# Kernel tuning notes

Measured on AMD Instinct MI355X. Metric: run time of the kernel, lower is better.

Reference implementation:

```python
import jax, jax.numpy as jnp
import numpy as np

N, D_IN, D_SAE, K = 8192, 768, 24576, 32


def setup_inputs() -> dict:
    key = jax.random.key(0)
    k1, k2, k3 = jax.random.split(key, 3)
    x = jax.random.normal(k1, (N, D_IN), dtype=jnp.float32)
    # kaiming_uniform_ on empty(d_in, d_sae): bound = sqrt(6 / d_in) (fan_in = d_sae? torch uses
    # fan_in = size(1) = d_sae for W_enc; we just need a same-scale random init for a reference)
    b_enc_bound = np.sqrt(6.0 / D_SAE)
    W_enc = jax.random.uniform(k2, (D_IN, D_SAE), dtype=jnp.float32,
                               minval=-b_enc_bound, maxval=b_enc_bound)
    b_dec_bound = np.sqrt(6.0 / D_IN)
    W_dec = jax.random.uniform(k3, (D_SAE, D_IN), dtype=jnp.float32,
                               minval=-b_dec_bound, maxval=b_dec_bound)
    # module normalizes decoder rows to unit L2 norm at init
    W_dec = W_dec / jnp.linalg.norm(W_dec, axis=1, keepdims=True)
    b_enc = jnp.zeros((D_SAE,), dtype=jnp.float32)
    b_dec = jnp.zeros((D_IN,), dtype=jnp.float32)
    return {"x": x, "W_enc": W_enc, "b_enc": b_enc, "W_dec": W_dec, "b_dec": b_dec}


def reference(x, W_enc, b_enc, W_dec, b_dec):
    # encode: relu((x - b_dec) @ W_enc + b_enc)
    z = jax.nn.relu((x - b_dec) @ W_enc + b_enc)            # [N, d_sae]
    topk_vals, topk_inds = jax.lax.top_k(z, K)              # [N, K]
    rows = jnp.arange(z.shape[0])[:, None]                  # [N, 1]
    z_sparse = jnp.zeros_like(z).at[rows, topk_inds].set(topk_vals)
    x_reconstruct = z_sparse @ W_dec + b_dec                # [N, d_in]
    return (x_reconstruct, z_sparse)
```

## Files before the change

### kernel.cpp

```cpp
#include <hip/hip_runtime.h>

#define N_ROWS 8192
#define D_IN   768
#define D_SAE  24576
#define K_TOP  32
#define C_SEL  40
#define DELTA  2e-4f

typedef __attribute__((ext_vector_type(8))) short bf16x8;
typedef __attribute__((ext_vector_type(4))) float f32x4;

__device__ __forceinline__ ushort f2bf(float f) {
    const unsigned u = __float_as_uint(f);
    return (ushort)((u + 0x7FFFu + ((u >> 16) & 1u)) >> 16);
}
__device__ __forceinline__ float bf2f(ushort h) {
    return __uint_as_float(((unsigned)h) << 16);
}

#define GBM 128
#define GBN 192
#define GBK 32

__global__ __launch_bounds__(256)
void sae_cvt_x(const float* __restrict__ x, const float* __restrict__ b_dec,
               ushort* __restrict__ ahi, ushort* __restrict__ alo)
{
    const int idx = blockIdx.x * 256 + threadIdx.x;
    const int i   = idx * 4;
    const int k   = (idx % (D_IN / 4)) * 4;
    const float4 xv = *(const float4*)(&x[i]);
    const float4 bd = *(const float4*)(&b_dec[k]);
    const float e[4] = {xv.x - bd.x, xv.y - bd.y, xv.z - bd.z, xv.w - bd.w};
    ushort h[4], l[4];
#pragma unroll
    for (int j = 0; j < 4; ++j) {
        h[j] = f2bf(e[j]);
        l[j] = f2bf(e[j] - bf2f(h[j]));
    }
    *(ushort4*)(&ahi[i]) = make_ushort4(h[0], h[1], h[2], h[3]);
    *(ushort4*)(&alo[i]) = make_ushort4(l[0], l[1], l[2], l[3]);
}

__global__ __launch_bounds__(256)
void sae_cvt_w(const float* __restrict__ W_enc,
               ushort* __restrict__ bhi, ushort* __restrict__ blo)
{
    __shared__ float tile[32][33];
    const int n0 = blockIdx.x * 32;
    const int k0 = blockIdx.y * 32;
    const int t  = threadIdx.x;
    const int r  = t >> 3;
    const int c4 = (t & 7) * 4;
    *(float4*)(&tile[r][c4]) = *(const float4*)(&W_enc[(size_t)(k0 + r) * D_SAE + n0 + c4]);
    __syncthreads();
    ushort h[4], l[4];
#pragma unroll
    for (int j = 0; j < 4; ++j) {
        const float e = tile[c4 + j][r];
        h[j] = f2bf(e);
        l[j] = f2bf(e - bf2f(h[j]));
    }
    *(ushort4*)(&bhi[(size_t)(n0 + r) * D_IN + k0 + c4]) = make_ushort4(h[0], h[1], h[2], h[3]);
    *(ushort4*)(&blo[(size_t)(n0 + r) * D_IN + k0 + c4]) = make_ushort4(l[0], l[1], l[2], l[3]);
}

__global__ __launch_bounds__(256, 2)
void sae_encode_mfma3(const ushort* __restrict__ ahi, const ushort* __restrict__ alo,
                      const ushort* __restrict__ bhi, const ushort* __restrict__ blo,
                      const float* __restrict__ b_enc, float* __restrict__ z)
{
    __shared__ ushort A_lds[2][4][GBM][8];
    __shared__ ushort B_lds[2][4][GBN][8];

    const int tid  = threadIdx.x;
    const int lane = tid & 63;
    const int wid  = tid >> 6;
    const int wr   = wid >> 1;
    const int wc   = wid & 1;
    const int l15  = lane & 15;
    const int lc   = lane >> 4;

    const int col0  = blockIdx.y * GBN;
    const int arow0 = blockIdx.x * GBM;
    const int row_w = arow0 + wr * 64;

    const int NT = D_IN / GBK;

    f32x4 acc[4][6];
#pragma unroll
    for (int i = 0; i < 4; ++i)
#pragma unroll
        for (int j = 0; j < 6; ++j) acc[i][j] = (f32x4){0.f, 0.f, 0.f, 0.f};

    bf16x8 s0, s1, s2, s3, s4, s5, s6, s7, s8, s9;

#define LOADQ(J, DST) { \
        const int q = (J) * 4 + wid; \
        if ((J) < 4) { \
            const int pl = q & 1, c = (q >> 1) & 3, h = q >> 3; \
            DST = *(const bf16x8*)((pl ? alo : ahi) + (size_t)(arow0 + h * 64 + lane) * D_IN + k0s + c * 8); \
        } else { \
            const int r2 = q - 16; \
            const int pl = r2 & 1, c = (r2 >> 1) & 3, g = r2 >> 3; \
            DST = *(const bf16x8*)((pl ? blo : bhi) + (size_t)(col0 + g * 64 + lane) * D_IN + k0s + c * 8); \
        } }

#define WRITEQ(J, SRC) { \
        const int q = (J) * 4 + wid; \
        if ((J) < 4) { \
            const int pl = q & 1, c = (q >> 1) & 3, h = q >> 3; \
            *(bf16x8*)(&A_lds[pl][c][h * 64 + lane][0]) = SRC; \
        } else { \
            const int r2 = q - 16; \
            const int pl = r2 & 1, c = (r2 >> 1) & 3, g = r2 >> 3; \
            *(bf16x8*)(&B_lds[pl][c][g * 64 + lane][0]) = SRC; \
        } }

#define LOAD_ALL() { LOADQ(0, s0) LOADQ(1, s1) LOADQ(2, s2) LOADQ(3, s3) LOADQ(4, s4) \
                     LOADQ(5, s5) LOADQ(6, s6) LOADQ(7, s7) LOADQ(8, s8) LOADQ(9, s9) }
#define WRITE_ALL() { WRITEQ(0, s0) WRITEQ(1, s1) WRITEQ(2, s2) WRITEQ(3, s3) WRITEQ(4, s4) \
                      WRITEQ(5, s5) WRITEQ(6, s6) WRITEQ(7, s7) WRITEQ(8, s8) WRITEQ(9, s9) }

    {
        const int k0s = 0;
        LOAD_ALL();
    }

    for (int kt = 0; kt < NT; ++kt) {
        WRITE_ALL();
        __syncthreads();

        if (kt + 1 < NT) {
            const int k0s = (kt + 1) * GBK;
            LOAD_ALL();
        }

        bf16x8 bh[6], bl[6];
#pragma unroll
        for (int ct = 0; ct < 6; ++ct) {
            const int n = wc * 96 + ct * 16 + l15;
            bh[ct] = *(const bf16x8*)(&B_lds[0][lc][n][0]);
            bl[ct] = *(const bf16x8*)(&B_lds[1][lc][n][0]);
        }
#pragma unroll
        for (int rt = 0; rt < 4; ++rt) {
            const int m = wr * 64 + rt * 16 + l15;
            const bf16x8 ah = *(const bf16x8*)(&A_lds[0][lc][m][0]);
            const bf16x8 al = *(const bf16x8*)(&A_lds[1][lc][m][0]);
#pragma unroll
            for (int ct = 0; ct < 6; ++ct) {
                acc[rt][ct] = __builtin_amdgcn_mfma_f32_16x16x32_bf16(ah, bh[ct], acc[rt][ct], 0, 0, 0);
                acc[rt][ct] = __builtin_amdgcn_mfma_f32_16x16x32_bf16(ah, bl[ct], acc[rt][ct], 0, 0, 0);
                acc[rt][ct] = __builtin_amdgcn_mfma_f32_16x16x32_bf16(al, bh[ct], acc[rt][ct], 0, 0, 0);
            }
        }
        __syncthreads();
    }

#undef LOAD_ALL
#undef WRITE_ALL
#undef LOADQ
#undef WRITEQ

#pragma unroll
    for (int ct = 0; ct < 6; ++ct) {
        const int col = col0 + wc * 96 + ct * 16 + l15;
        const float bec = b_enc[col];
#pragma unroll
        for (int rt = 0; rt < 4; ++rt) {
            const int rowb = row_w + rt * 16 + lc * 4;
#pragma unroll
            for (int r = 0; r < 4; ++r)
                z[(size_t)(rowb + r) * D_SAE + col] = fmaxf(acc[rt][ct][r] + bec, 0.f);
        }
    }
}

__global__ __launch_bounds__(256, 2)
void sae_encode_mfma(const float* __restrict__ x,
                     const float* __restrict__ W_enc,
                     const float* __restrict__ b_enc,
                     const float* __restrict__ b_dec,
                     float* __restrict__ z)
{
    __shared__ ushort Bs[2][4][GBN][8];

    const int tid  = threadIdx.x;
    const int lane = tid & 63;
    const int wid  = tid >> 6;
    const int wr   = wid >> 1;
    const int wc   = wid & 1;
    const int l15  = lane & 15;
    const int lc   = lane >> 4;

    const int col0  = blockIdx.x * GBN;
    const int row_w = blockIdx.y * GBM + wr * 64;

    f32x4 acc[4][6];
#pragma unroll
    for (int i = 0; i < 4; ++i)
#pragma unroll
        for (int j = 0; j < 6; ++j) acc[i][j] = (f32x4){0.f, 0.f, 0.f, 0.f};

    for (int kt = 0; kt < D_IN / GBK; ++kt) {
        const int k0 = kt * GBK;

        float bvv[3][8];
#pragma unroll
        for (int np = 0; np < 3; ++np)
#pragma unroll
            for (int it = 0; it < 8; ++it)
                bvv[np][it] = W_enc[(size_t)(k0 + wid * 8 + it) * D_SAE + col0 + np * 64 + lane];

        const float4 bd0 = *(const float4*)(&b_dec[k0 + lc * 8]);
        const float4 bd1 = *(const float4*)(&b_dec[k0 + lc * 8 + 4]);
        bf16x8 ah[4], al[4];
#pragma unroll
        for (int rt = 0; rt < 4; ++rt) {
            const size_t off = (size_t)(row_w + rt * 16 + l15) * D_IN + k0 + lc * 8;
            const float4 a0 = *(const float4*)(&x[off]);
            const float4 a1 = *(const float4*)(&x[off + 4]);
            float e[8];
            e[0] = a0.x - bd0.x; e[1] = a0.y - bd0.y; e[2] = a0.z - bd0.z; e[3] = a0.w - bd0.w;
            e[4] = a1.x - bd1.x; e[5] = a1.y - bd1.y; e[6] = a1.z - bd1.z; e[7] = a1.w - bd1.w;
#pragma unroll
            for (int j = 0; j < 8; ++j) {
                const ushort h = f2bf(e[j]);
                ah[rt][j] = (short)h;
                al[rt][j] = (short)f2bf(e[j] - bf2f(h));
            }
        }

        uint4 bh_pk[3], bl_pk[3];
#pragma unroll
        for (int np = 0; np < 3; ++np) {
            ushort h[8], l[8];
#pragma unroll
            for (int it = 0; it < 8; ++it) {
                h[it] = f2bf(bvv[np][it]);
                l[it] = f2bf(bvv[np][it] - bf2f(h[it]));
            }
            bh_pk[np] = make_uint4((unsigned)h[0] | ((unsigned)h[1] << 16),
                                   (unsigned)h[2] | ((unsigned)h[3] << 16),
                                   (unsigned)h[4] | ((unsigned)h[5] << 16),
                                   (unsigned)h[6] | ((unsigned)h[7] << 16));
            bl_pk[np] = make_uint4((unsigned)l[0] | ((unsigned)l[1] << 16),
                                   (unsigned)l[2] | ((unsigned)l[3] << 16),
                                   (unsigned)l[4] | ((unsigned)l[5] << 16),
                                   (unsigned)l[6] | ((unsigned)l[7] << 16));
        }

        __syncthreads();
#pragma unroll
        for (int np = 0; np < 3; ++np) {
            const int n = np * 64 + lane;
            *(uint4*)(&Bs[0][wid][n][0]) = bh_pk[np];
            *(uint4*)(&Bs[1][wid][n][0]) = bl_pk[np];
        }
        __syncthreads();

#pragma unroll
        for (int ct = 0; ct < 6; ++ct) {
            const int n = wc * 96 + ct * 16 + l15;
            const bf16x8 bh = *(const bf16x8*)(&Bs[0][lc][n][0]);
            const bf16x8 bl = *(const bf16x8*)(&Bs[1][lc][n][0]);
#pragma unroll
            for (int rt = 0; rt < 4; ++rt) {
                acc[rt][ct] = __builtin_amdgcn_mfma_f32_16x16x32_bf16(ah[rt], bh, acc[rt][ct], 0, 0, 0);
                acc[rt][ct] = __builtin_amdgcn_mfma_f32_16x16x32_bf16(ah[rt], bl, acc[rt][ct], 0, 0, 0);
                acc[rt][ct] = __builtin_amdgcn_mfma_f32_16x16x32_bf16(al[rt], bh, acc[rt][ct], 0, 0, 0);
            }
        }
    }

#pragma unroll
    for (int ct = 0; ct < 6; ++ct) {
        const int col = col0 + wc * 96 + ct * 16 + l15;
        const float bec = b_enc[col];
#pragma unroll
        for (int rt = 0; rt < 4; ++rt) {
            const int rowb = row_w + rt * 16 + lc * 4;
#pragma unroll
            for (int r = 0; r < 4; ++r)
                z[(size_t)(rowb + r) * D_SAE + col] = fmaxf(acc[rt][ct][r] + bec, 0.f);
        }
    }
}

#define TB     256
#define QPT    (D_SAE / 4 / TB)
#define HB     2048
#define NCOPY  2
#define BNDCAP 248
#define POOLN  288
#define NCAND  6
#define NEGF   -1e30f
#define BADIDX (1 << 30)

__global__ __launch_bounds__(TB, 4)
void sae_topk_decode(float* __restrict__ z,
                     const float* __restrict__ x,
                     const float* __restrict__ W_enc,
                     const float* __restrict__ b_enc,
                     const float* __restrict__ W_dec,
                     const float* __restrict__ b_dec,
                     float* __restrict__ x_rec)
{
    __shared__ int    hist[NCOPY * HB];
    __shared__ int    sufx[TB];
    __shared__ float  poolv[POOLN];
    __shared__ int    pooli[POOLN];
    __shared__ float  selv[C_SEL];
    __shared__ int    seli[C_SEL];
    __shared__ float  xrow[D_IN];
    __shared__ double cand[C_SEL];
    __shared__ int    shB, shChi;
    __shared__ int    nDef, nBnd, nFail;

    const int row = blockIdx.x;
    const int t   = threadIdx.x;
    const int w   = t >> 6;
    float* zr = z + (size_t)row * D_SAE;

    for (int i = t; i < NCOPY * HB; i += TB) hist[i] = 0;
    if (t == 0) { nDef = 0; nBnd = 0; nFail = 0; }
    __syncthreads();

    float cv[NCAND]; int ci[NCAND];
#pragma unroll
    for (int j = 0; j < NCAND; ++j) { cv[j] = NEGF; ci[j] = BADIDX; }
    {
        int* hw = &hist[(w >> 1) * HB];
        int zc = 0;
        for (int i0 = 0; i0 < QPT; i0 += 8) {
            f32x4 va[8];
#pragma unroll
            for (int u2 = 0; u2 < 8; ++u2)
                va[u2] = __builtin_nontemporal_load((const f32x4*)(&zr[(size_t)(t + (i0 + u2) * TB) * 4]));
#pragma unroll
            for (int u2 = 0; u2 < 8; ++u2) {
                const int base = (t + (i0 + u2) * TB) * 4;
#define PROC(f, o) { \
        const unsigned uu = __float_as_uint(f); \
        if (uu) atomicAdd(&hw[uu >> 20], 1); else ++zc; \
        const bool b0 = (f) > cv[0]; const bool b1 = (f) > cv[1]; const bool b2 = (f) > cv[2]; \
        const bool b3 = (f) > cv[3]; const bool b4 = (f) > cv[4]; const bool b5 = (f) > cv[5]; \
        if (b5) { \
            cv[5] = b4 ? cv[4] : (f);        ci[5] = b4 ? ci[4] : (base + o); \
            if (b4) { cv[4] = b3 ? cv[3] : (f); ci[4] = b3 ? ci[3] : (base + o); } \
            if (b3) { cv[3] = b2 ? cv[2] : (f); ci[3] = b2 ? ci[2] : (base + o); } \
            if (b2) { cv[2] = b1 ? cv[1] : (f); ci[2] = b1 ? ci[1] : (base + o); } \
            if (b1) { cv[1] = b0 ? cv[0] : (f); ci[1] = b0 ? ci[0] : (base + o); } \
            if (b0) { cv[0] = (f); ci[0] = (base + o); } \
        } }
                PROC(va[u2][0], 0) PROC(va[u2][1], 1) PROC(va[u2][2], 2) PROC(va[u2][3], 3)
#undef PROC
            }
        }
        if (zc) atomicAdd(&hw[0], zc);
    }
    __syncthreads();

    int cnt8[8]; int tot = 0;
#pragma unroll
    for (int j = 0; j < 8; ++j) {
        const int b = t * 8 + j;
        const int c = hist[b] + hist[HB + b];
        cnt8[j] = c; tot += c;
    }
    sufx[t] = tot;
    __syncthreads();
    for (int off = 1; off < TB; off <<= 1) {
        const int a = sufx[t];
        const int b = (t + off < TB) ? sufx[t + off] : 0;
        __syncthreads();
        sufx[t] = a + b;
        __syncthreads();
    }
    {
        int run = (t + 1 < TB) ? sufx[t + 1] : 0;
#pragma unroll
        for (int j = 7; j >= 0; --j) {
            const int c = cnt8[j];
            if (run < C_SEL && run + c >= C_SEL) { shB = t * 8 + j; shChi = run; }
            run += c;
        }
    }
    __syncthreads();
    const int B = shB;

    if (cv[NCAND - 1] > 0.f && (int)(__float_as_uint(cv[NCAND - 1]) >> 20) >= B) nFail = 1;
    __syncthreads();

    if (!nFail) {
#pragma unroll
        for (int j = 0; j < NCAND; ++j) {
            if (cv[j] > 0.f) {
                const int bk = (int)(__float_as_uint(cv[j]) >> 20);
                if (bk > B) {
                    const int p = atomicAdd(&nDef, 1);
                    poolv[p] = cv[j]; pooli[p] = ci[j];
                } else if (bk == B) {
                    const int p = atomicAdd(&nBnd, 1);
                    if (p < BNDCAP) { poolv[C_SEL + p] = cv[j]; pooli[C_SEL + p] = ci[j]; }
                }
            }
        }
    } else {
        for (int i = 0; i < QPT; ++i) {
            const float4 v = *(const float4*)(&zr[(size_t)(t + i * TB) * 4]);
            const int base = (t + i * TB) * 4;
#define COL(f, o) { const unsigned uu = __float_as_uint(f); if (uu) { const int bk = (int)(uu >> 20); \
            if (bk > B) { const int p = atomicAdd(&nDef, 1); poolv[p] = (f); pooli[p] = base + o; } \
            else if (bk == B) { const int p = atomicAdd(&nBnd, 1); if (p < BNDCAP) { poolv[C_SEL + p] = (f); pooli[C_SEL + p] = base + o; } } } }
            COL(v.x, 0) COL(v.y, 1) COL(v.z, 2) COL(v.w, 3)
#undef COL
        }
    }
    __syncthreads();

    {
        const int ndef  = nDef;
        const int nbndc = (nBnd < BNDCAP) ? nBnd : BNDCAP;
        for (int i = t; i < POOLN; i += TB)
            if (!(i < ndef) && !(i >= C_SEL && i < C_SEL + nbndc)) { poolv[i] = NEGF; pooli[i] = BADIDX; }
        if (t < C_SEL) { selv[t] = NEGF; seli[t] = BADIDX; }
    }
    __syncthreads();

    for (int e = t; e < POOLN; e += TB) {
        const float mv = poolv[e]; const int mi = pooli[e];
        int rank = 0;
        for (int j = 0; j < POOLN; ++j) {
            const float vj = poolv[j]; const int ij = pooli[j];
            if (vj > mv || (vj == mv && ij < mi)) ++rank;
        }
        if (rank < C_SEL && mi != BADIDX) { selv[rank] = mv; seli[rank] = mi; }
    }
    __syncthreads();

    if (selv[K_TOP - 1] - selv[K_TOP] < DELTA) {
        const int l = t & 63;
        for (int k = t; k < D_IN; k += TB) xrow[k] = x[(size_t)row * D_IN + k] - b_dec[k];
        __syncthreads();
        for (int j = w; j < C_SEL; j += 4) {
            const int c = seli[j];
            if (c < D_SAE) {
                double acc = 0.0;
#pragma unroll
                for (int q = 0; q < D_IN / 64; ++q) {
                    const int k = l + q * 64;
                    acc = fma((double)xrow[k], (double)W_enc[(size_t)k * D_SAE + c], acc);
                }
#pragma unroll
                for (int off = 32; off > 0; off >>= 1) acc += __shfl_down(acc, off);
                if (l == 0) {
                    const double vv = acc + (double)b_enc[c];
                    cand[j] = vv > 0.0 ? vv : 0.0;
                }
            } else if (l == 0) cand[j] = -1e300;
        }
        __syncthreads();
        if (t == 0) {
            bool used[C_SEL]; float nv[K_TOP]; int ni[K_TOP];
            for (int j = 0; j < C_SEL; ++j) used[j] = false;
            for (int s = 0; s < K_TOP; ++s) {
                int bj = -1; double bvv = 0.0; int bidx = 0;
                for (int j = 0; j < C_SEL; ++j) {
                    if (used[j]) continue;
                    const double v = cand[j]; const int idx = seli[j];
                    if (bj < 0 || v > bvv || (v == bvv && idx < bidx)) { bj = j; bvv = v; bidx = idx; }
                }
                used[bj] = true; nv[s] = (float)bvv; ni[s] = bidx;
            }
            for (int s = 0; s < K_TOP; ++s) { selv[s] = nv[s]; seli[s] = ni[s]; }
        }
        __syncthreads();
    }

    {
        const f32x4 z4 = (f32x4){0.f, 0.f, 0.f, 0.f};
        for (int i = 0; i < QPT; ++i)
            __builtin_nontemporal_store(z4, (f32x4*)(&zr[(size_t)(t + i * TB) * 4]));
    }
    __syncthreads();
    if (t < K_TOP && seli[t] < D_SAE) zr[seli[t]] = selv[t];

    float a0 = b_dec[t], a1 = b_dec[t + 256], a2 = b_dec[t + 512];
#pragma unroll 8
    for (int s = 0; s < K_TOP; ++s) {
        if (seli[s] < D_SAE) {
            const float v = selv[s];
            const float* wd = W_dec + (size_t)seli[s] * D_IN;
            a0 = fmaf(v, wd[t],       a0);
            a1 = fmaf(v, wd[t + 256], a1);
            a2 = fmaf(v, wd[t + 512], a2);
        }
    }
    float* xr = x_rec + (size_t)row * D_IN;
    xr[t] = a0; xr[t + 256] = a1; xr[t + 512] = a2;
}

extern "C" void kernel_launch(void* const* d_in, const int* in_sizes, int n_in,
                              void* d_out, int out_size, void* d_ws, size_t ws_size,
                              hipStream_t stream)
{
    const float* x     = (const float*)d_in[0];
    const float* W_enc = (const float*)d_in[1];
    const float* b_enc = (const float*)d_in[2];
    const float* W_dec = (const float*)d_in[3];
    const float* b_dec = (const float*)d_in[4];

    float* out   = (float*)d_out;
    float* x_rec = out;
    float* z     = out + (size_t)N_ROWS * D_IN;

    const size_t nA = (size_t)N_ROWS * D_IN;
    const size_t nB = (size_t)D_SAE * D_IN;
    const size_t need = (2 * nA + 2 * nB) * sizeof(ushort);

    if (ws_size >= need) {
        ushort* ahi = (ushort*)d_ws;
        ushort* alo = ahi + nA;
        ushort* bhi = alo + nA;
        ushort* blo = bhi + nB;
        sae_cvt_x<<<(int)(nA / 4 / 256), 256, 0, stream>>>(x, b_dec, ahi, alo);
        sae_cvt_w<<<dim3(D_SAE / 32, D_IN / 32), 256, 0, stream>>>(W_enc, bhi, blo);
        dim3 g1(N_ROWS / GBM, D_SAE / GBN);
        sae_encode_mfma3<<<g1, 256, 0, stream>>>(ahi, alo, bhi, blo, b_enc, z);
    } else {
        dim3 g0(D_SAE / GBN, N_ROWS / GBM);
        sae_encode_mfma<<<g0, 256, 0, stream>>>(x, W_enc, b_enc, b_dec, z);
    }
    sae_topk_decode<<<N_ROWS, TB, 0, stream>>>(z, x, W_enc, b_enc, W_dec, b_dec, x_rec);
}
```

Before: 2.140 ms.

## Build threshold histogram from per-thread candidates instead of every element

The per-element shared-memory histogram atomics in the main scan are removed. Instead, each thread adds only its top-NCAND candidates to the histogram, and the boundary bucket is chosen from that. If the boundary check fails, the full histogram is rebuilt with a second pass over the row. This cuts LDS atomic traffic in the hot loop but adds a costly fallback re-read when candidates don't cover the top set.

```diff
diff --git a/kernel.cpp b/kernel.cpp
--- a/kernel.cpp
+++ b/kernel.cpp
@@ -315,13 +315,14 @@
     __shared__ int    seli[C_SEL];
     __shared__ float  xrow[D_IN];
     __shared__ double cand[C_SEL];
-    __shared__ int    shB, shChi;
+    __shared__ int    shB;
     __shared__ int    nDef, nBnd, nFail;
 
     const int row = blockIdx.x;
     const int t   = threadIdx.x;
     const int w   = t >> 6;
     float* zr = z + (size_t)row * D_SAE;
+    int* hw = &hist[(w >> 1) * HB];
 
     for (int i = t; i < NCOPY * HB; i += TB) hist[i] = 0;
     if (t == 0) { nDef = 0; nBnd = 0; nFail = 0; }
@@ -331,8 +332,6 @@
 #pragma unroll
     for (int j = 0; j < NCAND; ++j) { cv[j] = NEGF; ci[j] = BADIDX; }
     {
-        int* hw = &hist[(w >> 1) * HB];
-        int zc = 0;
         for (int i0 = 0; i0 < QPT; i0 += 8) {
             f32x4 va[8];
 #pragma unroll
@@ -342,8 +341,6 @@
             for (int u2 = 0; u2 < 8; ++u2) {
                 const int base = (t + (i0 + u2) * TB) * 4;
 #define PROC(f, o) { \
-        const unsigned uu = __float_as_uint(f); \
-        if (uu) atomicAdd(&hw[uu >> 20], 1); else ++zc; \
         const bool b0 = (f) > cv[0]; const bool b1 = (f) > cv[1]; const bool b2 = (f) > cv[2]; \
         const bool b3 = (f) > cv[3]; const bool b4 = (f) > cv[4]; const bool b5 = (f) > cv[5]; \
         if (b5) { \
@@ -358,42 +355,83 @@
 #undef PROC
             }
         }
-        if (zc) atomicAdd(&hw[0], zc);
-    }
-    __syncthreads();
-
-    int cnt8[8]; int tot = 0;
-#pragma unroll
-    for (int j = 0; j < 8; ++j) {
-        const int b = t * 8 + j;
-        const int c = hist[b] + hist[HB + b];
-        cnt8[j] = c; tot += c;
-    }
-    sufx[t] = tot;
-    __syncthreads();
-    for (int off = 1; off < TB; off <<= 1) {
-        const int a = sufx[t];
-        const int b = (t + off < TB) ? sufx[t + off] : 0;
-        __syncthreads();
-        sufx[t] = a + b;
-        __syncthreads();
-    }
+    }
+
+#pragma unroll
+    for (int j = 0; j < NCAND; ++j)
+        atomicAdd(&hw[__float_as_uint(cv[j]) >> 20], 1);
+    __syncthreads();
+
     {
+        int cnt8[8]; int tot = 0;
+#pragma unroll
+        for (int j = 0; j < 8; ++j) {
+            const int b = t * 8 + j;
+            const int c = hist[b] + hist[HB + b];
+            cnt8[j] = c; tot += c;
+        }
+        sufx[t] = tot;
+        __syncthreads();
+        for (int off = 1; off < TB; off <<= 1) {
+            const int a = sufx[t];
+            const int b = (t + off < TB) ? sufx[t + off] : 0;
+            __syncthreads();
+            sufx[t] = a + b;
+            __syncthreads();
+        }
         int run = (t + 1 < TB) ? sufx[t + 1] : 0;
 #pragma unroll
         for (int j = 7; j >= 0; --j) {
             const int c = cnt8[j];
-            if (run < C_SEL && run + c >= C_SEL) { shB = t * 8 + j; shChi = run; }
+            if (run < C_SEL && run + c >= C_SEL) shB = t * 8 + j;
             run += c;
         }
     }
     __syncthreads();
+
+    if (cv[NCAND - 1] > 0.f && (int)(__float_as_uint(cv[NCAND - 1]) >> 20) >= shB) nFail = 1;
+    __syncthreads();
+    const bool fail = (nFail != 0);
+
+    if (fail) {
+        for (int i = t; i < NCOPY * HB; i += TB) hist[i] = 0;
+        __syncthreads();
+        for (int i = 0; i < QPT; ++i) {
+            const float4 v = *(const float4*)(&zr[(size_t)(t + i * TB) * 4]);
+            atomicAdd(&hw[__float_as_uint(v.x) >> 20], 1);
+            atomicAdd(&hw[__float_as_uint(v.y) >> 20], 1);
+            atomicAdd(&hw[__float_as_uint(v.z) >> 20], 1);
+            atomicAdd(&hw[__float_as_uint(v.w) >> 20], 1);
+        }
+        __syncthreads();
+        int cnt8[8]; int tot = 0;
+#pragma unroll
+        for (int j = 0; j < 8; ++j) {
+            const int b = t * 8 + j;
+            const int c = hist[b] + hist[HB + b];
+            cnt8[j] = c; tot += c;
+        }
+        sufx[t] = tot;
+        __syncthreads();
+        for (int off = 1; off < TB; off <<= 1) {
+            const int a = sufx[t];
+            const int b = (t + off < TB) ? sufx[t + off] : 0;
+            __syncthreads();
+            sufx[t] = a + b;
+            __syncthreads();
+        }
+        int run = (t + 1 < TB) ? sufx[t + 1] : 0;
+#pragma unroll
+        for (int j = 7; j >= 0; --j) {
+            const int c = cnt8[j];
+            if (run < C_SEL && run + c >= C_SEL) shB = t * 8 + j;
+            run += c;
+        }
+        __syncthreads();
+    }
     const int B = shB;
 
-    if (cv[NCAND - 1] > 0.f && (int)(__float_as_uint(cv[NCAND - 1]) >> 20) >= B) nFail = 1;
-    __syncthreads();
-
-    if (!nFail) {
+    if (!fail) {
 #pragma unroll
         for (int j = 0; j < NCAND; ++j) {
             if (cv[j] > 0.f) {
```

Result: no change. 2.130 ms (-0.4%).
